# Optimization experiments

Hardware: AMD Instinct MI355X
Metric: run time of the kernel (lower is better)

## Reference

```python
import jax, jax.numpy as jnp
import numpy as np

CH = 256          # channels
RED = 4           # reduction
C = CH // RED     # qk dim = 64
NCL = 128         # n_clusters
WIN = 144         # window_size
NR = 1            # n_rounds
RES = 0.1         # res_scale
EPS_N = 5e-05     # F.normalize eps used in attention path


def _norm(x, eps):
    # torch F.normalize semantics: x / max(||x||, eps)
    n = jnp.linalg.norm(x, axis=-1, keepdims=True)
    return x / jnp.maximum(n, eps)


def _conv(x, w, b, pad):
    y = jax.lax.conv_general_dilated(
        x, w, window_strides=(1, 1), padding=[(pad, pad), (pad, pad)],
        dimension_numbers=('NCHW', 'OIHW', 'NCHW'))
    return y + b[None, :, None, None]


def _add_adjacent(x):
    back = jnp.roll(x, 1, axis=2)
    fwd = jnp.roll(x, -1, axis=2)
    return jnp.concatenate([x, back, fwd], axis=3)


def setup_inputs() -> dict:
    key = jax.random.key(0)
    ks = jax.random.split(key, 5)
    N, H, W = 8, 96, 96
    return {
        'input_x': jax.random.normal(ks[0], (N, CH, H, W), jnp.float32),
        'means': jax.random.normal(ks[1], (NR, NCL, C), jnp.float32),
        'w_match': jax.random.normal(ks[2], (C, CH, 3, 3), jnp.float32) * 0.02,
        'b_match': jnp.zeros((C,), jnp.float32),
        'w_asm': jax.random.normal(ks[3], (CH, CH, 1, 1), jnp.float32) * 0.05,
        'b_asm': jnp.zeros((CH,), jnp.float32),
    }


def reference(input_x, means, w_match, b_match, w_asm, b_asm):
    N, ch, H, W = input_x.shape
    L = H * W
    nb = L // WIN

    # embeddings
    x_embed = _conv(input_x, w_match, b_match, 1).reshape(N, C, L).transpose(0, 2, 1)   # (N,L,C)
    y_embed = _conv(input_x, w_asm, b_asm, 0).reshape(N, ch, L).transpose(0, 2, 1)      # (N,L,ch)

    # kmeans bucket codes (no grad; int indices)
    xk = _norm(x_embed, 1e-12)[:, None]                      # (N,1,L,C) rounds expand
    dists = jnp.einsum('bhld,hcd->bhlc', xk, means)          # (N,NR,L,NCL)
    buckets = jnp.argmax(dists, axis=-1)                     # (N,NR,L)
    offsets = (jnp.arange(NR) * NCL).reshape(1, -1, 1)
    codes = (buckets + offsets).reshape(N, -1)               # (N, NR*L)

    indices = jnp.argsort(codes, axis=-1)
    undo_sort = jnp.argsort(indices, axis=-1)
    mod_indices = indices % L

    xs = jnp.take_along_axis(x_embed, mod_indices[..., None], axis=1)  # (N,NR*L,C)
    ys = jnp.take_along_axis(y_embed, mod_indices[..., None], axis=1)  # (N,NR*L,ch)

    xb = xs.reshape(N, NR, nb, WIN, C)
    yb = ys.reshape(N, NR, nb, WIN, ch)

    x_match = _add_adjacent(_norm(xb, EPS_N))
    yb3 = _add_adjacent(yb)

    raw = jnp.einsum('bhkie,bhkje->bhkij', xb, x_match)
    bscore = jax.scipy.special.logsumexp(raw, axis=-1, keepdims=True)
    score = jnp.exp(raw - bscore)

    ret = jnp.einsum('bukij,bukje->bukie', score, yb3)
    ret = ret.reshape(N, NR * L, ch)
    bs = bscore.reshape(N, NR * L)

    ret = jnp.take_along_axis(ret, undo_sort[..., None], axis=1)
    bs = jnp.take_along_axis(bs, undo_sort, axis=1)

    ret = ret.reshape(N, NR, L, ch)
    bs = bs.reshape(N, NR, L, 1)
    probs = jax.nn.softmax(bs, axis=1)                       # over rounds
    out = jnp.sum(ret * probs, axis=1)                       # (N,L,ch)

    out = out.transpose(0, 2, 1).reshape(N, ch, H, W) * RES + input_x
    return out
```

## Files before the change

kernel.cpp:

```cpp
#include <hip/hip_runtime.h>
#include <math.h>

typedef unsigned int u32;
typedef unsigned short u16;
typedef __bf16 bf16x8 __attribute__((ext_vector_type(8)));
typedef _Float16 f16x8 __attribute__((ext_vector_type(8)));
typedef float f32x4 __attribute__((ext_vector_type(4)));

#define LL 9216
#define WIN 144
#define NBK 64

__device__ __forceinline__ u16 f2bf(float f){
  union { float f; u32 u; } v; v.f = f;
  u32 u = v.u;
  return (u16)((u + 0x7fffu + ((u >> 16) & 1u)) >> 16);
}
__device__ __forceinline__ float bf2f(u16 b){
  union { u32 u; float f; } v; v.u = ((u32)b) << 16;
  return v.f;
}
__device__ __forceinline__ u16 f2h(float f){
  union { _Float16 h; u16 u; } v; v.h = (_Float16)f;
  return v.u;
}
__device__ __forceinline__ float h2f(u16 h){
  union { _Float16 h; u16 u; } v; v.u = h;
  return (float)v.h;
}
__device__ __forceinline__ f32x4 mfma16(bf16x8 a, bf16x8 b, f32x4 c){
  return __builtin_amdgcn_mfma_f32_16x16x32_bf16(a, b, c, 0, 0, 0);
}
__device__ __forceinline__ f32x4 mfma16h(f16x8 a, f16x8 b, f32x4 c){
  return __builtin_amdgcn_mfma_f32_16x16x32_f16(a, b, c, 0, 0, 0);
}

__global__ void __launch_bounds__(256) k_prep(const float* __restrict__ wm,
    const float* __restrict__ means, u16* __restrict__ WF16, float* __restrict__ MT){
  int i = blockIdx.x * 256 + threadIdx.x;
  if (i < 9*8*64*32){
    int tap = i >> 14;
    int cc  = (i >> 11) & 7;
    int o   = (i >> 5) & 63;
    int chl = i & 31;
    WF16[i] = f2h(wm[(o*256 + cc*32 + chl)*9 + tap]);
  }
  int j = i - 9*8*64*32;
  if (j >= 0 && j < 64*128){
    int d = j >> 7, cl = j & 127;
    MT[j] = means[cl*64 + d];
  }
}

__global__ void __launch_bounds__(256) k_xt(const float* __restrict__ x,
    u16* __restrict__ XTH, u16* __restrict__ XTL){
  __shared__ float ls[32][97];
  int hh = blockIdx.x, cc = blockIdx.y, n = blockIdx.z;
  int t = threadIdx.x;
  int h = hh - 1;
  bool interior = (h >= 0 && h < 96);
  if (interior){
    int c = t >> 3, w0 = (t & 7) * 12;
    const float* src = x + ((size_t)(n*256 + cc*32 + c))*9216 + h*96 + w0;
    float4 v0 = *(const float4*)src;
    float4 v1 = *(const float4*)(src + 4);
    float4 v2 = *(const float4*)(src + 8);
    ls[c][w0+0]=v0.x; ls[c][w0+1]=v0.y; ls[c][w0+2]=v0.z; ls[c][w0+3]=v0.w;
    ls[c][w0+4]=v1.x; ls[c][w0+5]=v1.y; ls[c][w0+6]=v1.z; ls[c][w0+7]=v1.w;
    ls[c][w0+8]=v2.x; ls[c][w0+9]=v2.y; ls[c][w0+10]=v2.z; ls[c][w0+11]=v2.w;
  }
  __syncthreads();
  size_t base = ((size_t)((n*8 + cc)*98 + hh))*3136;
  for (int u = t; u < 392; u += 256){
    int ww = u >> 2, s = u & 3;
    int w = ww - 1;
    u16 hbuf[8], lbuf[8];
    if (interior && w >= 0 && w < 96){
      int f = (ww >> 1) & 3;
      int cbase = (s ^ f) * 8;
      #pragma unroll
      for (int j = 0; j < 8; j++){
        float v = ls[cbase + j][w];
        _Float16 hv = (_Float16)v;
        float lres = v - (float)hv;
        union { _Float16 h; u16 u; } uh; uh.h = hv;
        hbuf[j] = uh.u;
        lbuf[j] = f2h(lres);
      }
    } else {
      #pragma unroll
      for (int j = 0; j < 8; j++){ hbuf[j] = 0; lbuf[j] = 0; }
    }
    *(uint4*)&XTH[base + ww*32 + s*8] = *(const uint4*)hbuf;
    *(uint4*)&XTL[base + ww*32 + s*8] = *(const uint4*)lbuf;
  }
}

__global__ void __launch_bounds__(256) k_conv3(
    const u16* __restrict__ XTH, const u16* __restrict__ XTL,
    const u16* __restrict__ WF16, const float* __restrict__ bm,
    float* __restrict__ XE){
  __shared__ u16 AH[3*3136];
  __shared__ u16 AL[3*3136];
  int h0 = blockIdx.x, n = blockIdx.y;
  int t = threadIdx.x;
  int wave = t >> 6, lane = t & 63, row = lane & 15, kg = lane >> 4;
  f32x4 acc[6];
  #pragma unroll
  for (int m = 0; m < 6; m++){ acc[m][0]=0.f; acc[m][1]=0.f; acc[m][2]=0.f; acc[m][3]=0.f; }
  for (int cc = 0; cc < 8; cc++){
    __syncthreads();
    const u16* srcH = XTH + ((size_t)((n*8 + cc)*98 + h0))*3136;
    const u16* srcL = XTL + ((size_t)((n*8 + cc)*98 + h0))*3136;
    for (int u = t; u < 1176; u += 256){
      *(uint4*)&AH[u*8] = *(const uint4*)&srcH[u*8];
      *(uint4*)&AL[u*8] = *(const uint4*)&srcL[u*8];
    }
    __syncthreads();
    #pragma unroll
    for (int dy = 0; dy < 3; dy++){
      #pragma unroll
      for (int dx = 0; dx < 3; dx++){
        const u16* wp = WF16 + (((size_t)((dy*3 + dx)*8 + cc)*64) + wave*16 + row)*32 + kg*8;
        f16x8 bfrag = *(const f16x8*)wp;
        #pragma unroll
        for (int mt = 0; mt < 6; mt++){
          int ww = mt*16 + row + dx;
          int sl = (kg ^ ((ww >> 1) & 3)) * 8;
          f16x8 ahi = *(const f16x8*)&AH[dy*3136 + ww*32 + sl];
          f16x8 alo = *(const f16x8*)&AL[dy*3136 + ww*32 + sl];
          acc[mt] = mfma16h(ahi, bfrag, acc[mt]);
          acc[mt] = mfma16h(alo, bfrag, acc[mt]);
        }
      }
    }
  }
  int o = wave*16 + row;
  float bb = bm[o];
  #pragma unroll
  for (int mt = 0; mt < 6; mt++){
    #pragma unroll
    for (int r = 0; r < 4; r++){
      int m = mt*16 + kg*4 + r;
      XE[((size_t)(n*9216 + h0*96 + m))*64 + o] = acc[mt][r] + bb;
    }
  }
}

__global__ void __launch_bounds__(256) k_dist(const float* __restrict__ XE,
    const float* __restrict__ MT, u32* __restrict__ CODE){
  __shared__ float ms[64][132];
  __shared__ float xsm[64][65];
  __shared__ float redv[64][16];
  __shared__ int  redi[64][16];
  int n = blockIdx.y, l0 = blockIdx.x * 64;
  int t = threadIdx.x;
  for (int e = t; e < 8192; e += 256) ms[e >> 7][e & 127] = MT[e];
  for (int e = t; e < 4096; e += 256)
    xsm[e >> 6][e & 63] = XE[((size_t)(n*9216 + l0 + (e >> 6)))*64 + (e & 63)];
  __syncthreads();
  int pg = t >> 4, cg = t & 15;
  int p0 = pg * 4, cl0 = cg * 8;
  float acc[4][8];
  #pragma unroll
  for (int i = 0; i < 4; i++)
    #pragma unroll
    for (int j = 0; j < 8; j++) acc[i][j] = 0.f;
  for (int d = 0; d < 64; d++){
    float4 m0 = *(const float4*)&ms[d][cl0];
    float4 m1 = *(const float4*)&ms[d][cl0 + 4];
    #pragma unroll
    for (int i = 0; i < 4; i++){
      float xv = xsm[p0 + i][d];
      acc[i][0] += xv * m0.x; acc[i][1] += xv * m0.y;
      acc[i][2] += xv * m0.z; acc[i][3] += xv * m0.w;
      acc[i][4] += xv * m1.x; acc[i][5] += xv * m1.y;
      acc[i][6] += xv * m1.z; acc[i][7] += xv * m1.w;
    }
  }
  #pragma unroll
  for (int i = 0; i < 4; i++){
    float bv = acc[i][0]; int bi = cl0;
    #pragma unroll
    for (int j = 1; j < 8; j++){ if (acc[i][j] > bv){ bv = acc[i][j]; bi = cl0 + j; } }
    redv[p0 + i][cg] = bv; redi[p0 + i][cg] = bi;
  }
  __syncthreads();
  if (t < 64){
    float bv = redv[t][0]; int bi = redi[t][0];
    for (int c = 1; c < 16; c++){
      float v = redv[t][c];
      if (v > bv){ bv = v; bi = redi[t][c]; }
    }
    CODE[n*9216 + l0 + t] = (u32)bi;
  }
}

__global__ void __launch_bounds__(256) k_sort(const u32* __restrict__ CODE,
    u32* __restrict__ IDX, u32* __restrict__ POS){
  __shared__ u32 hist[36][128];
  __shared__ u32 tot[128];
  __shared__ u32 whist[4][128];
  int n = blockIdx.x, t = threadIdx.x;
  for (int e = t; e < 36*128; e += 256) ((u32*)hist)[e] = 0;
  __syncthreads();
  for (int ch = 0; ch < 36; ch++){
    u32 c = CODE[n*9216 + ch*256 + t];
    atomicAdd(&hist[ch][c], 1u);
  }
  __syncthreads();
  if (t < 128){
    u32 run = 0;
    for (int ch = 0; ch < 36; ch++){ u32 v = hist[ch][t]; hist[ch][t] = run; run += v; }
    tot[t] = run;
  }
  __syncthreads();
  if (t == 0){
    u32 base = 0;
    for (int b = 0; b < 128; b++){ u32 v = tot[b]; tot[b] = base; base += v; }
  }
  __syncthreads();
  int wave = t >> 6, lane = t & 63;
  for (int ch = 0; ch < 36; ch++){
    for (int e = t; e < 512; e += 256) ((u32*)whist)[e] = 0;
    __syncthreads();
    int c = (int)CODE[n*9216 + ch*256 + t];
    atomicAdd(&whist[wave][c], 1u);
    __syncthreads();
    u32 pre = 0;
    for (int w2 = 0; w2 < wave; w2++) pre += whist[w2][c];
    u32 cnt = 0;
    for (int j = 0; j < 64; j++){
      int cj = __shfl(c, j, 64);
      cnt += (u32)((j < lane) && (cj == c));
    }
    u32 p = tot[c] + hist[ch][c] + pre + cnt;
    int l = ch*256 + t;
    IDX[n*9216 + p] = (u32)l;
    POS[n*9216 + l] = p;
    __syncthreads();
  }
}

__global__ void __launch_bounds__(256) k_conv1(const float* __restrict__ x,
    const float* __restrict__ wa, const float* __restrict__ ba,
    const u32* __restrict__ POS, u16* __restrict__ YS){
  __shared__ u16 As[64][40];
  __shared__ u16 Bs[256][40];
  __shared__ u16 rl[64][264];
  __shared__ u32 posl[64];
  int n = blockIdx.y, l0 = blockIdx.x * 64;
  int t = threadIdx.x;
  int wave = t >> 6, lane = t & 63, row = lane & 15, kg = lane >> 4;
  if (t < 64) posl[t] = POS[n*9216 + l0 + t];
  f32x4 acc[4][4];
  #pragma unroll
  for (int a = 0; a < 4; a++)
    #pragma unroll
    for (int b = 0; b < 4; b++){ acc[a][b][0]=0.f; acc[a][b][1]=0.f; acc[a][b][2]=0.f; acc[a][b][3]=0.f; }
  for (int ks = 0; ks < 8; ks++){
    int k0 = ks * 32;
    __syncthreads();
    for (int e = t; e < 64*32; e += 256){
      int ci = e >> 6, l = e & 63;
      As[l][ci] = f2bf(x[((size_t)(n*256 + k0 + ci))*9216 + l0 + l]);
    }
    for (int e = t; e < 256*32; e += 256){
      int co = e >> 5, ci = e & 31;
      Bs[co][ci] = f2bf(wa[co*256 + k0 + ci]);
    }
    __syncthreads();
    bf16x8 af[4], bfr[4];
    #pragma unroll
    for (int mt = 0; mt < 4; mt++) af[mt] = *(const bf16x8*)&As[mt*16 + row][kg*8];
    #pragma unroll
    for (int nt = 0; nt < 4; nt++) bfr[nt] = *(const bf16x8*)&Bs[wave*64 + nt*16 + row][kg*8];
    #pragma unroll
    for (int nt = 0; nt < 4; nt++)
      #pragma unroll
      for (int mt = 0; mt < 4; mt++)
        acc[mt][nt] = mfma16(af[mt], bfr[nt], acc[mt][nt]);
  }
  #pragma unroll
  for (int nt = 0; nt < 4; nt++){
    int co = wave*64 + nt*16 + row;
    float bb = ba[co];
    #pragma unroll
    for (int mt = 0; mt < 4; mt++)
      #pragma unroll
      for (int r = 0; r < 4; r++)
        rl[mt*16 + kg*4 + r][co] = f2bf(acc[mt][nt][r] + bb);
  }
  __syncthreads();
  for (int q = t; q < 64*32; q += 256){
    int r = q >> 5, part = q & 31;
    uint4 v = *(const uint4*)&rl[r][part*8];
    *(uint4*)&YS[((size_t)(n*9216 + (int)posl[r]))*256 + part*8] = v;
  }
}

__global__ void __launch_bounds__(256) k_gx(const float* __restrict__ XE,
    const u32* __restrict__ IDX, u16* __restrict__ XSN, float* __restrict__ RNRM){
  int gr = blockIdx.x * 4 + (threadIdx.x >> 6);
  int lane = threadIdx.x & 63;
  int n = gr / 9216;
  int l = (int)IDX[gr];
  float v = XE[((size_t)(n*9216 + l))*64 + lane];
  float s = v * v;
  #pragma unroll
  for (int m = 1; m < 64; m <<= 1) s += __shfl_xor(s, m, 64);
  float denom = fmaxf(sqrtf(s), 5e-5f);
  XSN[(size_t)gr*64 + lane] = f2bf(v / denom);
  if (lane == 0) RNRM[gr] = denom;
}

#define PL_STRIDE 456
#define SM_YLDS (144*456*2)
#define YL_STRIDE 20
#define SM_IDXL (SM_YLDS + 256*YL_STRIDE*4)
#define SM_ATTN (SM_IDXL + 144*4)

__global__ void __launch_bounds__(256, 1) k_attn(const u16* __restrict__ XSN,
    const u16* __restrict__ YS, const u32* __restrict__ IDX,
    const float* __restrict__ RNRM, u16* __restrict__ RET){
  extern __shared__ char smem[];
  u16* Plds = (u16*)smem;
  u32* Ylds = (u32*)(smem + SM_YLDS);
  u32* idxl = (u32*)(smem + SM_IDXL);
  int n = blockIdx.y, kw = blockIdx.x;
  int t = threadIdx.x;
  int wave = t >> 6, lane = t & 63;
  int row = lane & 15, kg = lane >> 4;
  int p0 = kw * WIN;
  if (t < WIN) idxl[t] = IDX[n*LL + p0 + t];
  int wprev = (kw + NBK - 1) & (NBK - 1), wnext = (kw + 1) & (NBK - 1);
  int segbase[3] = { p0, wprev*WIN, wnext*WIN };
  {
    bf16x8 a[9][2];
    #pragma unroll
    for (int mt = 0; mt < 9; mt++){
      const u16* xp = XSN + ((size_t)(n*LL + p0 + mt*16 + row))*64 + kg*8;
      a[mt][0] = *(const bf16x8*)xp;
      a[mt][1] = *(const bf16x8*)(xp + 32);
    }
    for (int jt = wave; jt < 27; jt += 4){
      int j0 = jt * 16;
      int seg = j0 / WIN;
      int sp = segbase[seg] + (j0 - seg*WIN) + row;
      const u16* bp = XSN + ((size_t)(n*LL + sp))*64 + kg*8;
      bf16x8 b0 = *(const bf16x8*)bp;
      bf16x8 b1 = *(const bf16x8*)(bp + 32);
      #pragma unroll
      for (int mt = 0; mt < 9; mt++){
        f32x4 s; s[0]=0.f; s[1]=0.f; s[2]=0.f; s[3]=0.f;
        s = mfma16(a[mt][0], b0, s);
        s = mfma16(a[mt][1], b1, s);
        #pragma unroll
        for (int r = 0; r < 4; r++)
          Plds[(mt*16 + kg*4 + r)*PL_STRIDE + j0 + row] = f2bf(s[r]);
      }
    }
  }
  __syncthreads();
  for (int pass = 0; pass < 9; pass++){
    int rr = pass*16 + (t >> 4);
    int tc = t & 15;
    float rn = RNRM[n*LL + p0 + rr];
    u16* prow = Plds + rr*PL_STRIDE;
    float vals[27]; float mx = -1e30f;
    #pragma unroll
    for (int jj = 0; jj < 27; jj++){ vals[jj] = bf2f(prow[tc + 16*jj]) * rn; mx = fmaxf(mx, vals[jj]); }
    mx = fmaxf(mx, __shfl_xor(mx, 1, 64));
    mx = fmaxf(mx, __shfl_xor(mx, 2, 64));
    mx = fmaxf(mx, __shfl_xor(mx, 4, 64));
    mx = fmaxf(mx, __shfl_xor(mx, 8, 64));
    float sum = 0.f;
    #pragma unroll
    for (int jj = 0; jj < 27; jj++){ vals[jj] = __expf(vals[jj] - mx); sum += vals[jj]; }
    sum += __shfl_xor(sum, 1, 64);
    sum += __shfl_xor(sum, 2, 64);
    sum += __shfl_xor(sum, 4, 64);
    sum += __shfl_xor(sum, 8, 64);
    float inv = 1.f / sum;
    #pragma unroll
    for (int jj = 0; jj < 27; jj++) prow[tc + 16*jj] = f2bf(vals[jj] * inv);
    if (tc < 12){ prow[432 + tc] = 0; prow[444 + tc] = 0; }
  }
  __syncthreads();
  f32x4 acc[9][4];
  #pragma unroll
  for (int a = 0; a < 9; a++)
    #pragma unroll
    for (int b = 0; b < 4; b++){ acc[a][b][0]=0.f; acc[a][b][1]=0.f; acc[a][b][2]=0.f; acc[a][b][3]=0.f; }
  for (int ks = 0; ks < 14; ks++){
    int j0 = ks * 32;
    __syncthreads();
    for (int it = t; it < 512; it += 256){
      int q = it & 15;
      int c8 = (it >> 4) * 8;
      int jA = j0 + 2*q;
      if (jA >= 432){
        #pragma unroll
        for (int kk = 0; kk < 8; kk++) Ylds[(c8 + kk)*YL_STRIDE + q] = 0u;
      } else {
        int seg = jA / WIN;
        int spA = segbase[seg] + (jA - seg*WIN);
        const u16* ya = YS + ((size_t)(n*LL + spA))*256 + c8;
        uint4 va = *(const uint4*)ya;
        uint4 vb = *(const uint4*)(ya + 256);
        u32 pa[4] = {va.x, va.y, va.z, va.w};
        u32 pb[4] = {vb.x, vb.y, vb.z, vb.w};
        #pragma unroll
        for (int kk = 0; kk < 4; kk++){
          Ylds[(c8 + 2*kk    )*YL_STRIDE + q] = (pa[kk] & 0xffffu) | (pb[kk] << 16);
          Ylds[(c8 + 2*kk + 1)*YL_STRIDE + q] = (pa[kk] >> 16) | (pb[kk] & 0xffff0000u);
        }
      }
    }
    __syncthreads();
    bf16x8 ap[9];
    #pragma unroll
    for (int mt = 0; mt < 9; mt++)
      ap[mt] = *(const bf16x8*)&Plds[(mt*16 + row)*PL_STRIDE + j0 + kg*8];
    #pragma unroll
    for (int nt = 0; nt < 4; nt++){
      int co = (wave*4 + nt)*16 + row;
      bf16x8 bv = *(const bf16x8*)&Ylds[co*YL_STRIDE + kg*4];
      #pragma unroll
      for (int mt = 0; mt < 9; mt++)
        acc[mt][nt] = mfma16(ap[mt], bv, acc[mt][nt]);
    }
  }
  __syncthreads();
  u16* rstage = Plds;
  #pragma unroll
  for (int mt = 0; mt < 9; mt++)
    #pragma unroll
    for (int nt = 0; nt < 4; nt++){
      int co = (wave*4 + nt)*16 + row;
      #pragma unroll
      for (int r = 0; r < 4; r++)
        rstage[(mt*16 + kg*4 + r)*264 + co] = f2bf(acc[mt][nt][r]);
    }
  __syncthreads();
  for (int q = t; q < WIN*32; q += 256){
    int rr2 = q >> 5, part = q & 31;
    uint4 v = *(const uint4*)&rstage[rr2*264 + part*8];
    *(uint4*)&RET[((size_t)(n*LL + (int)idxl[rr2]))*256 + part*8] = v;
  }
}

__global__ void __launch_bounds__(256) k_final(const u16* __restrict__ RET,
    const float* __restrict__ x, float* __restrict__ out){
  __shared__ u16 tl[64][72];
  int n = blockIdx.z, cb = blockIdx.y * 64, l0 = blockIdx.x * 64;
  int t = threadIdx.x;
  for (int it = t; it < 512; it += 256){
    int r = it >> 3, part = it & 7;
    uint4 v = *(const uint4*)&RET[((size_t)(n*9216 + l0 + r))*256 + cb + part*8];
    *(uint4*)&tl[r][part*8] = v;
  }
  __syncthreads();
  int col = t >> 2, lq = (t & 3) * 16;
  int co = cb + col;
  const float* xin = x + ((size_t)(n*256 + co))*9216 + l0 + lq;
  float* op = out + ((size_t)(n*256 + co))*9216 + l0 + lq;
  #pragma unroll
  for (int i4 = 0; i4 < 4; i4++){
    float4 o4;
    o4.x = fmaf(bf2f(tl[lq + i4*4 + 0][col]), 0.1f, xin[i4*4 + 0]);
    o4.y = fmaf(bf2f(tl[lq + i4*4 + 1][col]), 0.1f, xin[i4*4 + 1]);
    o4.z = fmaf(bf2f(tl[lq + i4*4 + 2][col]), 0.1f, xin[i4*4 + 2]);
    o4.w = fmaf(bf2f(tl[lq + i4*4 + 3][col]), 0.1f, xin[i4*4 + 3]);
    *(float4*)&op[i4*4] = o4;
  }
}

#define OFF_XE   ((size_t)0)
#define SZ_XE    (8ull*9216*64*4)
#define OFF_WF   (OFF_XE + SZ_XE)
#define SZ_WF    (9ull*8*64*32*2)
#define OFF_MT   (OFF_WF + SZ_WF)
#define SZ_MT    (64ull*128*4)
#define OFF_CODE (OFF_MT + SZ_MT)
#define SZ_CODE  (8ull*9216*4)
#define OFF_IDX  (OFF_CODE + SZ_CODE)
#define OFF_POS  (OFF_IDX + SZ_CODE)
#define OFF_XSN  (OFF_POS + SZ_CODE)
#define SZ_XSN   (8ull*9216*64*2)
#define OFF_RNRM (OFF_XSN + SZ_XSN)
#define SZ_RNRM  (8ull*9216*4)
#define OFF_XTH  (OFF_RNRM + SZ_RNRM)
#define SZ_XTP   (8ull*8*98*98*32*2 + 32768)
#define OFF_XTL  (OFF_XTH + SZ_XTP)

extern "C" void kernel_launch(void* const* d_in, const int* in_sizes, int n_in,
                              void* d_out, int out_size, void* d_ws, size_t ws_size,
                              hipStream_t stream){
  const float* x     = (const float*)d_in[0];
  const float* means = (const float*)d_in[1];
  const float* wm    = (const float*)d_in[2];
  const float* bm    = (const float*)d_in[3];
  const float* wa    = (const float*)d_in[4];
  const float* ba    = (const float*)d_in[5];
  float* out = (float*)d_out;
  char* ws = (char*)d_ws;

  float* XE   = (float*)(ws + OFF_XE);
  u16*   WF16 = (u16*)(ws + OFF_WF);
  float* MT   = (float*)(ws + OFF_MT);
  u32*   CODE = (u32*)(ws + OFF_CODE);
  u32*   IDX  = (u32*)(ws + OFF_IDX);
  u32*   POS  = (u32*)(ws + OFF_POS);
  u16*   XSN  = (u16*)(ws + OFF_XSN);
  float* RNRM = (float*)(ws + OFF_RNRM);
  u16*   XTH  = (u16*)(ws + OFF_XTH);
  u16*   XTL  = (u16*)(ws + OFF_XTL);
  u16*   YS   = (u16*)(ws + OFF_XTH);
  u16*   RET  = (u16*)(ws + OFF_XTL);

  hipFuncSetAttribute((const void*)k_attn,
                      hipFuncAttributeMaxDynamicSharedMemorySize, SM_ATTN);

  k_prep <<<608, 256, 0, stream>>>(wm, means, WF16, MT);
  k_xt   <<<dim3(98, 8, 8), 256, 0, stream>>>(x, XTH, XTL);
  k_conv3<<<dim3(96, 8), 256, 0, stream>>>(XTH, XTL, WF16, bm, XE);
  k_dist <<<dim3(144, 8), 256, 0, stream>>>(XE, MT, CODE);
  k_sort <<<8, 256, 0, stream>>>(CODE, IDX, POS);
  k_conv1<<<dim3(144, 8), 256, 0, stream>>>(x, wa, ba, POS, YS);
  k_gx   <<<18432, 256, 0, stream>>>(XE, IDX, XSN, RNRM);
  k_attn <<<dim3(64, 8), 256, SM_ATTN, stream>>>(XSN, YS, IDX, RNRM, RET);
  k_final<<<dim3(144, 4, 8), 256, 0, stream>>>(RET, x, out);
}
```

Before: 578.2 us.

## Pre-pack 1x1 conv operands into bf16 MFMA fragment layout and enlarge tiles

Adds a k_xb kernel that converts the input to bf16 packed as 8-channel groups per pixel, and extends k_prep to pre-pack the 1x1 weights the same way. k_conv1 now loads MFMA fragments straight from global memory, with no LDS staging or per-iteration barriers. Each block now covers 128 pixels instead of 64, and the scatter of results is done in two halves. The cost is an extra pass over the input and a larger register footprint for the accumulators.

```diff
diff --git a/kernel.cpp b/kernel.cpp
--- a/kernel.cpp
+++ b/kernel.cpp
@@ -24,10 +24,6 @@
   union { _Float16 h; u16 u; } v; v.h = (_Float16)f;
   return v.u;
 }
-__device__ __forceinline__ float h2f(u16 h){
-  union { _Float16 h; u16 u; } v; v.u = h;
-  return (float)v.h;
-}
 __device__ __forceinline__ f32x4 mfma16(bf16x8 a, bf16x8 b, f32x4 c){
   return __builtin_amdgcn_mfma_f32_16x16x32_bf16(a, b, c, 0, 0, 0);
 }
@@ -36,7 +32,8 @@
 }
 
 __global__ void __launch_bounds__(256) k_prep(const float* __restrict__ wm,
-    const float* __restrict__ means, u16* __restrict__ WF16, float* __restrict__ MT){
+    const float* __restrict__ means, const float* __restrict__ wa,
+    u16* __restrict__ WF16, float* __restrict__ MT, u16* __restrict__ WB){
   int i = blockIdx.x * 256 + threadIdx.x;
   if (i < 9*8*64*32){
     int tap = i >> 14;
@@ -49,6 +46,13 @@
   if (j >= 0 && j < 64*128){
     int d = j >> 7, cl = j & 127;
     MT[j] = means[cl*64 + d];
+  }
+  int j2 = j - 64*128;
+  if (j2 >= 0 && j2 < 32*256*8){
+    int c8 = j2 >> 11;
+    int rest = j2 & 2047;
+    int o = rest >> 3, jj = rest & 7;
+    WB[j2] = f2bf(wa[o*256 + c8*8 + jj]);
   }
 }
 
@@ -147,6 +151,17 @@
   }
 }
 
+__global__ void __launch_bounds__(256) k_xb(const float* __restrict__ x,
+    u16* __restrict__ XB){
+  int l = blockIdx.x * 256 + threadIdx.x;
+  int c8 = blockIdx.y, n = blockIdx.z;
+  const float* xp = x + ((size_t)(n*256 + c8*8))*9216 + l;
+  u16 buf[8];
+  #pragma unroll
+  for (int j = 0; j < 8; j++) buf[j] = f2bf(xp[(size_t)j*9216]);
+  *(uint4*)&XB[(((size_t)(n*32 + c8))*9216 + l)*8] = *(const uint4*)buf;
+}
+
 __global__ void __launch_bounds__(256) k_dist(const float* __restrict__ XE,
     const float* __restrict__ MT, u32* __restrict__ CODE){
   __shared__ float ms[64][132];
@@ -242,60 +257,58 @@
   }
 }
 
-__global__ void __launch_bounds__(256) k_conv1(const float* __restrict__ x,
-    const float* __restrict__ wa, const float* __restrict__ ba,
+__global__ void __launch_bounds__(256) k_conv1(const u16* __restrict__ XB,
+    const u16* __restrict__ WB, const float* __restrict__ ba,
     const u32* __restrict__ POS, u16* __restrict__ YS){
-  __shared__ u16 As[64][40];
-  __shared__ u16 Bs[256][40];
   __shared__ u16 rl[64][264];
-  __shared__ u32 posl[64];
-  int n = blockIdx.y, l0 = blockIdx.x * 64;
+  __shared__ u32 posl[128];
+  int n = blockIdx.y, l0 = blockIdx.x * 128;
   int t = threadIdx.x;
-  int wave = t >> 6, lane = t & 63, row = lane & 15, kg = lane >> 4;
-  if (t < 64) posl[t] = POS[n*9216 + l0 + t];
-  f32x4 acc[4][4];
-  #pragma unroll
-  for (int a = 0; a < 4; a++)
+  int wv = t >> 6, lane = t & 63, row = lane & 15, kg = lane >> 4;
+  if (t < 128) posl[t] = POS[n*9216 + l0 + t];
+  f32x4 acc[8][4];
+  #pragma unroll
+  for (int a = 0; a < 8; a++)
     #pragma unroll
     for (int b = 0; b < 4; b++){ acc[a][b][0]=0.f; acc[a][b][1]=0.f; acc[a][b][2]=0.f; acc[a][b][3]=0.f; }
+  const u16* xbase = XB + (((size_t)(n*32 + kg))*9216 + l0 + row)*8;
+  const u16* wbase = WB + (((size_t)kg*256) + wv*64 + row)*8;
   for (int ks = 0; ks < 8; ks++){
-    int k0 = ks * 32;
-    __syncthreads();
-    for (int e = t; e < 64*32; e += 256){
-      int ci = e >> 6, l = e & 63;
-      As[l][ci] = f2bf(x[((size_t)(n*256 + k0 + ci))*9216 + l0 + l]);
-    }
-    for (int e = t; e < 256*32; e += 256){
-      int co = e >> 5, ci = e & 31;
-      Bs[co][ci] = f2bf(wa[co*256 + k0 + ci]);
-    }
-    __syncthreads();
-    bf16x8 af[4], bfr[4];
-    #pragma unroll
-    for (int mt = 0; mt < 4; mt++) af[mt] = *(const bf16x8*)&As[mt*16 + row][kg*8];
-    #pragma unroll
-    for (int nt = 0; nt < 4; nt++) bfr[nt] = *(const bf16x8*)&Bs[wave*64 + nt*16 + row][kg*8];
+    const u16* xp = xbase + (size_t)ks*4*9216*8;
+    const u16* wp = wbase + (size_t)ks*4*256*8;
+    bf16x8 a[8], b[4];
+    #pragma unroll
+    for (int mt = 0; mt < 8; mt++) a[mt] = *(const bf16x8*)(xp + mt*128);
+    #pragma unroll
+    for (int nt = 0; nt < 4; nt++) b[nt] = *(const bf16x8*)(wp + nt*128);
     #pragma unroll
     for (int nt = 0; nt < 4; nt++)
       #pragma unroll
-      for (int mt = 0; mt < 4; mt++)
-        acc[mt][nt] = mfma16(af[mt], bfr[nt], acc[mt][nt]);
-  }
-  #pragma unroll
-  for (int nt = 0; nt < 4; nt++){
-    int co = wave*64 + nt*16 + row;
-    float bb = ba[co];
-    #pragma unroll
-    for (int mt = 0; mt < 4; mt++)
-      #pragma unroll
-      for (int r = 0; r < 4; r++)
-        rl[mt*16 + kg*4 + r][co] = f2bf(acc[mt][nt][r] + bb);
-  }
-  __syncthreads();
-  for (int q = t; q < 64*32; q += 256){
-    int r = q >> 5, part = q & 31;
-    uint4 v = *(const uint4*)&rl[r][part*8];
-    *(uint4*)&YS[((size_t)(n*9216 + (int)posl[r]))*256 + part*8] = v;
+      for (int mt = 0; mt < 8; mt++)
+        acc[mt][nt] = mfma16(a[mt], b[nt], acc[mt][nt]);
+  }
+  float bb[4];
+  #pragma unroll
+  for (int nt = 0; nt < 4; nt++) bb[nt] = ba[wv*64 + nt*16 + row];
+  #pragma unroll
+  for (int half = 0; half < 2; half++){
+    __syncthreads();
+    #pragma unroll
+    for (int m4 = 0; m4 < 4; m4++){
+      #pragma unroll
+      for (int nt = 0; nt < 4; nt++){
+        int co = wv*64 + nt*16 + row;
+        #pragma unroll
+        for (int r = 0; r < 4; r++)
+          rl[m4*16 + kg*4 + r][co] = f2bf(acc[half*4 + m4][nt][r] + bb[nt]);
+      }
+    }
+    __syncthreads();
+    for (int q = t; q < 2048; q += 256){
+      int r = q >> 5, part = q & 31;
+      uint4 v = *(const uint4*)&rl[r][part*8];
+      *(uint4*)&YS[((size_t)(n*9216 + (int)posl[half*64 + r]))*256 + part*8] = v;
+    }
   }
 }
 
@@ -482,7 +495,9 @@
 #define SZ_WF    (9ull*8*64*32*2)
 #define OFF_MT   (OFF_WF + SZ_WF)
 #define SZ_MT    (64ull*128*4)
-#define OFF_CODE (OFF_MT + SZ_MT)
+#define OFF_WB   (OFF_MT + SZ_MT)
+#define SZ_WB    (32ull*256*8*2)
+#define OFF_CODE (OFF_WB + SZ_WB)
 #define SZ_CODE  (8ull*9216*4)
 #define OFF_IDX  (OFF_CODE + SZ_CODE)
 #define OFF_POS  (OFF_IDX + SZ_CODE)
@@ -509,6 +524,7 @@
   float* XE   = (float*)(ws + OFF_XE);
   u16*   WF16 = (u16*)(ws + OFF_WF);
   float* MT   = (float*)(ws + OFF_MT);
+  u16*   WB   = (u16*)(ws + OFF_WB);
   u32*   CODE = (u32*)(ws + OFF_CODE);
   u32*   IDX  = (u32*)(ws + OFF_IDX);
   u32*   POS  = (u32*)(ws + OFF_POS);
@@ -517,17 +533,19 @@
   u16*   XTH  = (u16*)(ws + OFF_XTH);
   u16*   XTL  = (u16*)(ws + OFF_XTL);
   u16*   YS   = (u16*)(ws + OFF_XTH);
+  u16*   XB   = (u16*)(ws + OFF_XTL);
   u16*   RET  = (u16*)(ws + OFF_XTL);
 
   hipFuncSetAttribute((const void*)k_attn,
                       hipFuncAttributeMaxDynamicSharedMemorySize, SM_ATTN);
 
-  k_prep <<<608, 256, 0, stream>>>(wm, means, WF16, MT);
+  k_prep <<<864, 256, 0, stream>>>(wm, means, wa, WF16, MT, WB);
   k_xt   <<<dim3(98, 8, 8), 256, 0, stream>>>(x, XTH, XTL);
   k_conv3<<<dim3(96, 8), 256, 0, stream>>>(XTH, XTL, WF16, bm, XE);
+  k_xb   <<<dim3(36, 32, 8), 256, 0, stream>>>(x, XB);
   k_dist <<<dim3(144, 8), 256, 0, stream>>>(XE, MT, CODE);
   k_sort <<<8, 256, 0, stream>>>(CODE, IDX, POS);
-  k_conv1<<<dim3(144, 8), 256, 0, stream>>>(x, wa, ba, POS, YS);
+  k_conv1<<<dim3(72, 8), 256, 0, stream>>>(XB, WB, ba, POS, YS);
   k_gx   <<<18432, 256, 0, stream>>>(XE, IDX, XSN, RNRM);
   k_attn <<<dim3(64, 8), 256, SM_ATTN, stream>>>(XSN, YS, IDX, RNRM, RET);
   k_final<<<dim3(144, 4, 8), 256, 0, stream>>>(RET, x, out);
```

Result: faster. 513.2 us (-11.2%).
